# Kernel tuning notes

Hardware: AMD Instinct MI355X
Metric: run time of the kernel (lower is better)

The kernel has to match this reference:

```python
import jax, jax.numpy as jnp
import numpy as np

N, C, H, W = 512, 2048, 16, 8
NUM_CLASSES = 751
ALPHA = 1.2      # margin
LAMB = 0.5       # self.l
SIGMA = 0.8      # osm_sigma
BN_EPS = 1e-5


def setup_inputs() -> dict:
    key = jax.random.key(0)
    k1, k2, k3 = jax.random.split(key, 3)
    features = jax.random.normal(k1, (N, C, H, W), dtype=jnp.float32)
    targets = jax.random.randint(k2, (N,), 0, NUM_CLASSES)
    gamma = jnp.ones((C,), dtype=jnp.float32)  # BN weight, init 1 (weights_init_kaiming)
    # kaiming_uniform_(a=sqrt(5)) on [NUM_CLASSES, C]: bound = 1/sqrt(C)
    bound = 1.0 / np.sqrt(C)
    weight = jax.random.uniform(k3, (NUM_CLASSES, C), jnp.float32, -bound, bound)
    return {"features": features, "targets": targets, "gamma": gamma, "weight": weight}


def _l2norm(x, axis=-1):
    return x / jnp.maximum(jnp.linalg.norm(x, axis=axis, keepdims=True), 1e-12)


def reference(features, targets, gamma, weight):
    n = features.shape[0]
    # AdaptiveAvgPool2d(1) + Flatten
    global_feat = jnp.mean(features, axis=(2, 3))  # [n, C]
    # NoBiasBatchNorm1d (training mode: batch stats, biased var, no bias)
    mu = jnp.mean(global_feat, axis=0)
    var = jnp.var(global_feat, axis=0)
    bn_feat = (global_feat - mu) / jnp.sqrt(var + BN_EPS) * gamma
    bn_feat = _l2norm(bn_feat, axis=1)  # F.normalize

    # pairwise euclidean distance
    sq = jnp.sum(bn_feat * bn_feat, axis=1)                       # [n]
    dist2 = sq[:, None] + sq[None, :] - 2.0 * (bn_feat @ bn_feat.T)
    dist = jnp.sqrt(jnp.clip(dist2, 1e-12, None))                 # [n, n]

    S_pos = jnp.exp(-(dist * dist) / (SIGMA * SIGMA))
    S_neg = jnp.clip(ALPHA - dist, 1e-12, None)
    p_mask = targets[:, None] == targets[None, :]                 # [n, n] bool
    S = jnp.where(p_mask, S_pos, S_neg)

    # per-sample attention: exp(logits)[i, t_i] / sum_j exp(logits)[i, j] == softmax
    logits = bn_feat @ _l2norm(weight, axis=1).T                  # [n, num_classes]
    probs = jax.nn.softmax(logits, axis=1)
    atten = probs[jnp.arange(n), targets]                         # [n]
    A = jnp.minimum(atten[None, :], atten[:, None])               # [n, n]

    Wmat = S * A
    off_diag = 1.0 - jnp.eye(n, dtype=Wmat.dtype)
    W_P = Wmat * p_mask.astype(Wmat.dtype) * off_diag
    W_N = Wmat * (~p_mask).astype(Wmat.dtype) * off_diag

    L_P = 0.5 * jnp.sum(W_P * dist * dist) / jnp.sum(W_P)
    L_N = 0.5 * jnp.sum(W_N * S_neg * S_neg) / jnp.sum(W_N)
    L = (1.0 - LAMB) * L_P + LAMB * L_N
    return (L, global_feat)
```

## Files before the change

### kernel.cpp

```cpp
#include <hip/hip_runtime.h>
#include <hip/hip_bf16.h>
#include <math.h>

#define N_S   512
#define C_S   2048
#define HW_S  128
#define NCLS  751
#define NCLSP 768
#define ALPHA 1.2f
#define LAMB  0.5f
#define SIGMA 0.8f
#define BN_EPS 1e-5f

typedef __attribute__((ext_vector_type(8))) short short8;
typedef __attribute__((ext_vector_type(4))) float f32x4;

__device__ __forceinline__ unsigned short f2bf(float x) {
    __hip_bfloat16 h = __float2bfloat16(x);
    return *reinterpret_cast<unsigned short*>(&h);
}

__global__ __launch_bounds__(256) void pool_kernel(const float* __restrict__ feat,
                                                   float* __restrict__ out_gf,
                                                   float* __restrict__ accum) {
    if (blockIdx.x == 0 && threadIdx.x < 8) accum[threadIdx.x] = 0.0f;
    int pair = blockIdx.x * 16 + (threadIdx.x >> 4);
    int sub  = threadIdx.x & 15;
    const float4* p = reinterpret_cast<const float4*>(feat + (size_t)pair * HW_S);
    float4 v0 = p[sub];
    float4 v1 = p[sub + 16];
    float s = (v0.x + v0.y + v0.z + v0.w) + (v1.x + v1.y + v1.z + v1.w);
    #pragma unroll
    for (int off = 8; off > 0; off >>= 1) s += __shfl_down(s, off, 16);
    if (sub == 0) out_gf[pair] = s * (1.0f / HW_S);
}

__global__ __launch_bounds__(256) void meanvar_kernel(const float* __restrict__ gf,
                                                      const float* __restrict__ gamma,
                                                      float* __restrict__ mu_out,
                                                      float* __restrict__ scale_out) {
    int tc = threadIdx.x & 31;
    int tr = threadIdx.x >> 5;
    int c  = blockIdx.x * 32 + tc;
    const float* col = gf + c;
    float sum = 0.f, sumsq = 0.f;
    #pragma unroll 4
    for (int n = tr * 64; n < tr * 64 + 64; ++n) {
        float x = col[(size_t)n * C_S];
        sum += x; sumsq += x * x;
    }
    __shared__ float s1[8][32], s2[8][32];
    s1[tr][tc] = sum; s2[tr][tc] = sumsq;
    __syncthreads();
    if (threadIdx.x < 32) {
        int cc = blockIdx.x * 32 + threadIdx.x;
        float a = 0.f, b = 0.f;
        #pragma unroll
        for (int r = 0; r < 8; ++r) { a += s1[r][threadIdx.x]; b += s2[r][threadIdx.x]; }
        float mu  = a * (1.0f / N_S);
        float var = b * (1.0f / N_S) - mu * mu;
        mu_out[cc]    = mu;
        scale_out[cc] = gamma[cc] / sqrtf(var + BN_EPS);
    }
}

__global__ __launch_bounds__(256) void bnnorm_kernel(const float* __restrict__ gf,
                                                     const float* __restrict__ mu,
                                                     const float* __restrict__ scale,
                                                     unsigned short* __restrict__ bnnh,
                                                     float* __restrict__ sq) {
    int n = blockIdx.x, t = threadIdx.x;
    const float* row = gf + (size_t)n * C_S;
    float v[8];
    float ss = 0.f;
    #pragma unroll
    for (int k = 0; k < 8; ++k) {
        int c = t + k * 256;
        float x = (row[c] - mu[c]) * scale[c];
        v[k] = x; ss += x * x;
    }
    __shared__ float red[4];
    __shared__ float sinv;
    #pragma unroll
    for (int off = 32; off > 0; off >>= 1) ss += __shfl_down(ss, off, 64);
    if ((t & 63) == 0) red[t >> 6] = ss;
    __syncthreads();
    if (t == 0) {
        float tot = red[0] + red[1] + red[2] + red[3];
        float inv = 1.0f / fmaxf(sqrtf(tot), 1e-12f);
        sinv  = inv;
        sq[n] = tot * inv * inv;
    }
    __syncthreads();
    float inv = sinv;
    unsigned short* orow = bnnh + (size_t)n * C_S;
    #pragma unroll
    for (int k = 0; k < 8; ++k) orow[t + k * 256] = f2bf(v[k] * inv);
}

__global__ __launch_bounds__(256) void wnorm_kernel(const float* __restrict__ w,
                                                    unsigned short* __restrict__ wnh) {
    int kcls = blockIdx.x, t = threadIdx.x;
    unsigned short* orow = wnh + (size_t)kcls * C_S;
    if (kcls >= NCLS) {
        #pragma unroll
        for (int k = 0; k < 8; ++k) orow[t + k * 256] = 0;
        return;
    }
    const float* row = w + (size_t)kcls * C_S;
    float v[8];
    float ss = 0.f;
    #pragma unroll
    for (int k = 0; k < 8; ++k) {
        float x = row[t + k * 256];
        v[k] = x; ss += x * x;
    }
    __shared__ float red[4];
    __shared__ float sinv;
    #pragma unroll
    for (int off = 32; off > 0; off >>= 1) ss += __shfl_down(ss, off, 64);
    if ((t & 63) == 0) red[t >> 6] = ss;
    __syncthreads();
    if (t == 0) sinv = 1.0f / fmaxf(sqrtf(red[0] + red[1] + red[2] + red[3]), 1e-12f);
    __syncthreads();
    float inv = sinv;
    #pragma unroll
    for (int k = 0; k < 8; ++k) orow[t + k * 256] = f2bf(v[k] * inv);
}

__global__ __launch_bounds__(64) void mfma_gemm_nt(const unsigned short* __restrict__ Ah,
                                                   const unsigned short* __restrict__ Bh,
                                                   float* __restrict__ Cm,
                                                   int K, int ldc) {
    int lane = threadIdx.x & 63;
    int m0 = blockIdx.x * 16;
    int n0 = blockIdx.y * 64;
    int mrow = m0 + (lane & 15);
    int kq   = (lane >> 4) * 8;
    f32x4 acc0 = {0.f,0.f,0.f,0.f}, acc1 = {0.f,0.f,0.f,0.f};
    f32x4 acc2 = {0.f,0.f,0.f,0.f}, acc3 = {0.f,0.f,0.f,0.f};
    const unsigned short* arow = Ah + (size_t)mrow * K + kq;
    const unsigned short* brow = Bh + (size_t)(n0 + (lane & 15)) * K + kq;
    #pragma unroll 2
    for (int k = 0; k < K; k += 32) {
        short8 a  = *reinterpret_cast<const short8*>(arow + k);
        short8 b0 = *reinterpret_cast<const short8*>(brow + k);
        short8 b1 = *reinterpret_cast<const short8*>(brow + 16 * K + k);
        short8 b2 = *reinterpret_cast<const short8*>(brow + 32 * K + k);
        short8 b3 = *reinterpret_cast<const short8*>(brow + 48 * K + k);
        acc0 = __builtin_amdgcn_mfma_f32_16x16x32_bf16(a, b0, acc0, 0, 0, 0);
        acc1 = __builtin_amdgcn_mfma_f32_16x16x32_bf16(a, b1, acc1, 0, 0, 0);
        acc2 = __builtin_amdgcn_mfma_f32_16x16x32_bf16(a, b2, acc2, 0, 0, 0);
        acc3 = __builtin_amdgcn_mfma_f32_16x16x32_bf16(a, b3, acc3, 0, 0, 0);
    }
    int ccol  = lane & 15;
    int crow0 = m0 + (lane >> 4) * 4;
    #pragma unroll
    for (int r = 0; r < 4; ++r) {
        float* orow = Cm + (size_t)(crow0 + r) * ldc + n0 + ccol;
        orow[0]  = acc0[r];
        orow[16] = acc1[r];
        orow[32] = acc2[r];
        orow[48] = acc3[r];
    }
}

__global__ __launch_bounds__(256) void softmax_atten_kernel(const float* __restrict__ logits,
                                                            const int* __restrict__ targets,
                                                            float* __restrict__ atten) {
    int n = blockIdx.x, t = threadIdx.x;
    const float* row = logits + (size_t)n * NCLSP;
    __shared__ float red[4];
    __shared__ float srmax, srsum;
    float m = -1e30f;
    for (int k = t; k < NCLS; k += 256) m = fmaxf(m, row[k]);
    #pragma unroll
    for (int off = 32; off > 0; off >>= 1) m = fmaxf(m, __shfl_down(m, off, 64));
    if ((t & 63) == 0) red[t >> 6] = m;
    __syncthreads();
    if (t == 0) srmax = fmaxf(fmaxf(red[0], red[1]), fmaxf(red[2], red[3]));
    __syncthreads();
    float rm = srmax;
    float s = 0.f;
    for (int k = t; k < NCLS; k += 256) s += expf(row[k] - rm);
    #pragma unroll
    for (int off = 32; off > 0; off >>= 1) s += __shfl_down(s, off, 64);
    if ((t & 63) == 0) red[t >> 6] = s;
    __syncthreads();
    if (t == 0) {
        srsum = red[0] + red[1] + red[2] + red[3];
        atten[n] = expf(row[targets[n]] - rm) / srsum;
    }
}

__global__ __launch_bounds__(256) void pair_reduce_kernel(const float* __restrict__ G,
                                                          const float* __restrict__ sq,
                                                          const float* __restrict__ atten,
                                                          const int* __restrict__ targets,
                                                          float* __restrict__ accum,
                                                          float* __restrict__ out) {
    float numP = 0.f, denP = 0.f, numN = 0.f, denN = 0.f;
    const float inv_sig2 = 1.0f / (SIGMA * SIGMA);
    for (int p = blockIdx.x * 256 + threadIdx.x; p < N_S * N_S; p += 256 * 256) {
        int i = p >> 9, j = p & (N_S - 1);
        if (i == j) continue;
        float d2   = fmaxf(sq[i] + sq[j] - 2.0f * G[p], 1e-12f);
        float dist = sqrtf(d2);
        float sneg = fmaxf(ALPHA - dist, 1e-12f);
        float Aij  = fminf(atten[i], atten[j]);
        if (targets[i] == targets[j]) {
            float Wm = expf(-d2 * inv_sig2) * Aij;
            numP += Wm * d2; denP += Wm;
        } else {
            float Wm = sneg * Aij;
            numN += Wm * sneg * sneg; denN += Wm;
        }
    }
    #pragma unroll
    for (int off = 32; off > 0; off >>= 1) {
        numP += __shfl_down(numP, off, 64);
        denP += __shfl_down(denP, off, 64);
        numN += __shfl_down(numN, off, 64);
        denN += __shfl_down(denN, off, 64);
    }
    __shared__ float red[4][4];
    int t = threadIdx.x;
    if ((t & 63) == 0) {
        int w = t >> 6;
        red[w][0] = numP; red[w][1] = denP; red[w][2] = numN; red[w][3] = denN;
    }
    __syncthreads();
    if (t < 4) {
        float s = red[0][t] + red[1][t] + red[2][t] + red[3][t];
        atomicAdd(&accum[t], s);
    }
    __syncthreads();
    if (t == 0) {
        __threadfence();
        unsigned prev = atomicAdd(reinterpret_cast<unsigned*>(accum + 4), 1u);
        if (prev == gridDim.x - 1) {
            float a0 = atomicAdd(&accum[0], 0.0f);
            float a1 = atomicAdd(&accum[1], 0.0f);
            float a2 = atomicAdd(&accum[2], 0.0f);
            float a3 = atomicAdd(&accum[3], 0.0f);
            float L_P = 0.5f * a0 / a1;
            float L_N = 0.5f * a2 / a3;
            out[0] = (1.0f - LAMB) * L_P + LAMB * L_N;
        }
    }
}

extern "C" void kernel_launch(void* const* d_in, const int* in_sizes, int n_in,
                              void* d_out, int out_size, void* d_ws, size_t ws_size,
                              hipStream_t stream) {
    const float* features = (const float*)d_in[0];
    const int*   targets  = (const int*)d_in[1];
    const float* gamma    = (const float*)d_in[2];
    const float* weight   = (const float*)d_in[3];
    float* out = (float*)d_out;
    float* gf  = out + 1;

    float* ws     = (float*)d_ws;
    float* mu     = ws;
    float* scale  = mu + 2048;
    float* sq     = scale + 2048;
    float* atten  = sq + 512;
    float* accum  = atten + 512;
    float* logits = accum + 8;
    float* G      = logits + 393216;
    unsigned short* bnnh = (unsigned short*)(G + 262144);
    unsigned short* wnh  = bnnh + 1048576;

    hipLaunchKernelGGL(pool_kernel, dim3((N_S * C_S) / 16), dim3(256), 0, stream,
                       features, gf, accum);
    hipLaunchKernelGGL(meanvar_kernel, dim3(C_S / 32), dim3(256), 0, stream,
                       gf, gamma, mu, scale);
    hipLaunchKernelGGL(bnnorm_kernel, dim3(N_S), dim3(256), 0, stream,
                       gf, mu, scale, bnnh, sq);
    hipLaunchKernelGGL(wnorm_kernel, dim3(NCLSP), dim3(256), 0, stream, weight, wnh);
    hipLaunchKernelGGL(mfma_gemm_nt, dim3(N_S / 16, NCLSP / 64), dim3(64), 0, stream,
                       bnnh, wnh, logits, C_S, NCLSP);
    hipLaunchKernelGGL(softmax_atten_kernel, dim3(N_S), dim3(256), 0, stream,
                       logits, targets, atten);
    hipLaunchKernelGGL(mfma_gemm_nt, dim3(N_S / 16, N_S / 64), dim3(64), 0, stream,
                       bnnh, bnnh, G, C_S, N_S);
    hipLaunchKernelGGL(pair_reduce_kernel, dim3(256), dim3(256), 0, stream,
                       G, sq, atten, targets, accum, out);
}
```

Before: 746.9 us.

## Fuse post-pool stages into one persistent kernel with grid barriers

Replaces six separate kernel launches (mean/var, BN normalize, weight normalize, two GEMMs, softmax, pair reduce) with a single persistent kernel of 512 blocks that uses atomic-counter grid barriers between phases. Both GEMMs now run concurrently in one phase, and the pair reduction uses twice as many blocks. The aim is to remove launch overhead and inter-kernel gaps. The cost is spin-wait barriers, which rely on all 512 blocks being co-resident and can deadlock otherwise. Phases with fewer tasks than blocks also leave hardware idle.

```diff
diff --git a/kernel.cpp b/kernel.cpp
--- a/kernel.cpp
+++ b/kernel.cpp
@@ -11,6 +11,7 @@
 #define LAMB  0.5f
 #define SIGMA 0.8f
 #define BN_EPS 1e-5f
+#define NBLK  512
 
 typedef __attribute__((ext_vector_type(8))) short short8;
 typedef __attribute__((ext_vector_type(4))) float f32x4;
@@ -22,8 +23,8 @@
 
 __global__ __launch_bounds__(256) void pool_kernel(const float* __restrict__ feat,
                                                    float* __restrict__ out_gf,
-                                                   float* __restrict__ accum) {
-    if (blockIdx.x == 0 && threadIdx.x < 8) accum[threadIdx.x] = 0.0f;
+                                                   float* __restrict__ ctrl) {
+    if (blockIdx.x == 0 && threadIdx.x < 16) ctrl[threadIdx.x] = 0.0f;
     int pair = blockIdx.x * 16 + (threadIdx.x >> 4);
     int sub  = threadIdx.x & 15;
     const float4* p = reinterpret_cast<const float4*>(feat + (size_t)pair * HW_S);
@@ -35,217 +36,231 @@
     if (sub == 0) out_gf[pair] = s * (1.0f / HW_S);
 }
 
-__global__ __launch_bounds__(256) void meanvar_kernel(const float* __restrict__ gf,
-                                                      const float* __restrict__ gamma,
-                                                      float* __restrict__ mu_out,
-                                                      float* __restrict__ scale_out) {
-    int tc = threadIdx.x & 31;
-    int tr = threadIdx.x >> 5;
-    int c  = blockIdx.x * 32 + tc;
-    const float* col = gf + c;
-    float sum = 0.f, sumsq = 0.f;
-    #pragma unroll 4
-    for (int n = tr * 64; n < tr * 64 + 64; ++n) {
-        float x = col[(size_t)n * C_S];
-        sum += x; sumsq += x * x;
-    }
-    __shared__ float s1[8][32], s2[8][32];
-    s1[tr][tc] = sum; s2[tr][tc] = sumsq;
+__device__ __forceinline__ void grid_bar(unsigned* __restrict__ bars, int idx) {
     __syncthreads();
-    if (threadIdx.x < 32) {
-        int cc = blockIdx.x * 32 + threadIdx.x;
-        float a = 0.f, b = 0.f;
+    if (threadIdx.x == 0) {
+        __threadfence();
+        atomicAdd(&bars[idx], 1u);
+        while (atomicAdd(&bars[idx], 0u) < NBLK) __builtin_amdgcn_s_sleep(1);
+        __threadfence();
+    }
+    __syncthreads();
+}
+
+__global__ __launch_bounds__(256, 2) void fused_kernel(
+        const float* __restrict__ gf, const float* __restrict__ gamma,
+        const float* __restrict__ weight, const int* __restrict__ targets,
+        float* __restrict__ mu, float* __restrict__ scale,
+        float* __restrict__ sq, float* __restrict__ atten,
+        float* __restrict__ logits, float* __restrict__ G,
+        unsigned short* __restrict__ bnnh, unsigned short* __restrict__ wnh,
+        float* __restrict__ ctrl, float* __restrict__ out) {
+    const int t = threadIdx.x;
+    const int b = blockIdx.x;
+    unsigned* bars = reinterpret_cast<unsigned*>(ctrl + 8);
+
+    __shared__ float red1[8][32];
+    __shared__ float red2[8][32];
+    __shared__ float sred[4];
+    __shared__ float sbc[2];
+
+    if (b < 64) {
+        int tc = t & 31, tr = t >> 5;
+        int c = b * 32 + tc;
+        const float* col = gf + c;
+        float sum = 0.f, sumsq = 0.f;
+        #pragma unroll 4
+        for (int n = tr * 64; n < tr * 64 + 64; ++n) {
+            float x = col[(size_t)n * C_S];
+            sum += x; sumsq += x * x;
+        }
+        red1[tr][tc] = sum; red2[tr][tc] = sumsq;
+        __syncthreads();
+        if (t < 32) {
+            float a = 0.f, bb = 0.f;
+            #pragma unroll
+            for (int r = 0; r < 8; ++r) { a += red1[r][t]; bb += red2[r][t]; }
+            int cc = b * 32 + t;
+            float m   = a * (1.0f / N_S);
+            float var = bb * (1.0f / N_S) - m * m;
+            mu[cc]    = m;
+            scale[cc] = gamma[cc] / sqrtf(var + BN_EPS);
+        }
+    }
+    grid_bar(bars, 0);
+
+    for (int task = b; task < N_S + NCLSP; task += NBLK) {
+        __syncthreads();
+        if (task < N_S) {
+            int n = task;
+            const float* row = gf + (size_t)n * C_S;
+            float v[8]; float ss = 0.f;
+            #pragma unroll
+            for (int k = 0; k < 8; ++k) {
+                int c = t + k * 256;
+                float x = (row[c] - mu[c]) * scale[c];
+                v[k] = x; ss += x * x;
+            }
+            #pragma unroll
+            for (int off = 32; off > 0; off >>= 1) ss += __shfl_down(ss, off, 64);
+            if ((t & 63) == 0) sred[t >> 6] = ss;
+            __syncthreads();
+            if (t == 0) {
+                float tot = sred[0] + sred[1] + sred[2] + sred[3];
+                float inv = 1.0f / fmaxf(sqrtf(tot), 1e-12f);
+                sbc[0] = inv;
+                sq[n]  = tot * inv * inv;
+            }
+            __syncthreads();
+            float inv = sbc[0];
+            unsigned short* orow = bnnh + (size_t)n * C_S;
+            #pragma unroll
+            for (int k = 0; k < 8; ++k) orow[t + k * 256] = f2bf(v[k] * inv);
+        } else {
+            int r = task - N_S;
+            unsigned short* orow = wnh + (size_t)r * C_S;
+            if (r >= NCLS) {
+                #pragma unroll
+                for (int k = 0; k < 8; ++k) orow[t + k * 256] = 0;
+            } else {
+                const float* row = weight + (size_t)r * C_S;
+                float v[8]; float ss = 0.f;
+                #pragma unroll
+                for (int k = 0; k < 8; ++k) {
+                    float x = row[t + k * 256];
+                    v[k] = x; ss += x * x;
+                }
+                #pragma unroll
+                for (int off = 32; off > 0; off >>= 1) ss += __shfl_down(ss, off, 64);
+                if ((t & 63) == 0) sred[t >> 6] = ss;
+                __syncthreads();
+                if (t == 0) sbc[0] = 1.0f / fmaxf(sqrtf(sred[0]+sred[1]+sred[2]+sred[3]), 1e-12f);
+                __syncthreads();
+                float inv = sbc[0];
+                #pragma unroll
+                for (int k = 0; k < 8; ++k) orow[t + k * 256] = f2bf(v[k] * inv);
+            }
+        }
+    }
+    grid_bar(bars, 1);
+
+    {
+        int wave = t >> 6, lane = t & 63;
+        int gid = b * 4 + wave;
+        if (gid < 640) {
+            const unsigned short* Ah = bnnh;
+            const unsigned short* Bh; float* Cm; int m0, n0, ldc;
+            if (gid < 384) {
+                Bh = wnh;  Cm = logits; m0 = (gid & 31) * 16; n0 = (gid >> 5) * 64; ldc = NCLSP;
+            } else {
+                int g2 = gid - 384;
+                Bh = bnnh; Cm = G;      m0 = (g2 & 31) * 16;  n0 = (g2 >> 5) * 64;  ldc = N_S;
+            }
+            int mrow = m0 + (lane & 15);
+            int kq   = (lane >> 4) * 8;
+            f32x4 acc0 = {0,0,0,0}, acc1 = {0,0,0,0}, acc2 = {0,0,0,0}, acc3 = {0,0,0,0};
+            const unsigned short* arow = Ah + (size_t)mrow * C_S + kq;
+            const unsigned short* brow = Bh + (size_t)(n0 + (lane & 15)) * C_S + kq;
+            #pragma unroll 2
+            for (int k = 0; k < C_S; k += 32) {
+                short8 a  = *reinterpret_cast<const short8*>(arow + k);
+                short8 b0 = *reinterpret_cast<const short8*>(brow + k);
+                short8 b1 = *reinterpret_cast<const short8*>(brow + 16 * C_S + k);
+                short8 b2 = *reinterpret_cast<const short8*>(brow + 32 * C_S + k);
+                short8 b3 = *reinterpret_cast<const short8*>(brow + 48 * C_S + k);
+                acc0 = __builtin_amdgcn_mfma_f32_16x16x32_bf16(a, b0, acc0, 0, 0, 0);
+                acc1 = __builtin_amdgcn_mfma_f32_16x16x32_bf16(a, b1, acc1, 0, 0, 0);
+                acc2 = __builtin_amdgcn_mfma_f32_16x16x32_bf16(a, b2, acc2, 0, 0, 0);
+                acc3 = __builtin_amdgcn_mfma_f32_16x16x32_bf16(a, b3, acc3, 0, 0, 0);
+            }
+            int ccol  = lane & 15;
+            int crow0 = m0 + (lane >> 4) * 4;
+            #pragma unroll
+            for (int r = 0; r < 4; ++r) {
+                float* orow = Cm + (size_t)(crow0 + r) * ldc + n0 + ccol;
+                orow[0]  = acc0[r];
+                orow[16] = acc1[r];
+                orow[32] = acc2[r];
+                orow[48] = acc3[r];
+            }
+        }
+    }
+    grid_bar(bars, 2);
+
+    {
+        int n = b;
+        const float* row = logits + (size_t)n * NCLSP;
+        float m = -1e30f;
+        for (int k = t; k < NCLS; k += 256) m = fmaxf(m, row[k]);
         #pragma unroll
-        for (int r = 0; r < 8; ++r) { a += s1[r][threadIdx.x]; b += s2[r][threadIdx.x]; }
-        float mu  = a * (1.0f / N_S);
-        float var = b * (1.0f / N_S) - mu * mu;
-        mu_out[cc]    = mu;
-        scale_out[cc] = gamma[cc] / sqrtf(var + BN_EPS);
-    }
-}
-
-__global__ __launch_bounds__(256) void bnnorm_kernel(const float* __restrict__ gf,
-                                                     const float* __restrict__ mu,
-                                                     const float* __restrict__ scale,
-                                                     unsigned short* __restrict__ bnnh,
-                                                     float* __restrict__ sq) {
-    int n = blockIdx.x, t = threadIdx.x;
-    const float* row = gf + (size_t)n * C_S;
-    float v[8];
-    float ss = 0.f;
-    #pragma unroll
-    for (int k = 0; k < 8; ++k) {
-        int c = t + k * 256;
-        float x = (row[c] - mu[c]) * scale[c];
-        v[k] = x; ss += x * x;
-    }
-    __shared__ float red[4];
-    __shared__ float sinv;
-    #pragma unroll
-    for (int off = 32; off > 0; off >>= 1) ss += __shfl_down(ss, off, 64);
-    if ((t & 63) == 0) red[t >> 6] = ss;
-    __syncthreads();
-    if (t == 0) {
-        float tot = red[0] + red[1] + red[2] + red[3];
-        float inv = 1.0f / fmaxf(sqrtf(tot), 1e-12f);
-        sinv  = inv;
-        sq[n] = tot * inv * inv;
-    }
-    __syncthreads();
-    float inv = sinv;
-    unsigned short* orow = bnnh + (size_t)n * C_S;
-    #pragma unroll
-    for (int k = 0; k < 8; ++k) orow[t + k * 256] = f2bf(v[k] * inv);
-}
-
-__global__ __launch_bounds__(256) void wnorm_kernel(const float* __restrict__ w,
-                                                    unsigned short* __restrict__ wnh) {
-    int kcls = blockIdx.x, t = threadIdx.x;
-    unsigned short* orow = wnh + (size_t)kcls * C_S;
-    if (kcls >= NCLS) {
+        for (int off = 32; off > 0; off >>= 1) m = fmaxf(m, __shfl_down(m, off, 64));
+        if ((t & 63) == 0) sred[t >> 6] = m;
+        __syncthreads();
+        if (t == 0) sbc[0] = fmaxf(fmaxf(sred[0], sred[1]), fmaxf(sred[2], sred[3]));
+        __syncthreads();
+        float rm = sbc[0];
+        float s = 0.f;
+        for (int k = t; k < NCLS; k += 256) s += expf(row[k] - rm);
         #pragma unroll
-        for (int k = 0; k < 8; ++k) orow[t + k * 256] = 0;
-        return;
-    }
-    const float* row = w + (size_t)kcls * C_S;
-    float v[8];
-    float ss = 0.f;
-    #pragma unroll
-    for (int k = 0; k < 8; ++k) {
-        float x = row[t + k * 256];
-        v[k] = x; ss += x * x;
-    }
-    __shared__ float red[4];
-    __shared__ float sinv;
-    #pragma unroll
-    for (int off = 32; off > 0; off >>= 1) ss += __shfl_down(ss, off, 64);
-    if ((t & 63) == 0) red[t >> 6] = ss;
-    __syncthreads();
-    if (t == 0) sinv = 1.0f / fmaxf(sqrtf(red[0] + red[1] + red[2] + red[3]), 1e-12f);
-    __syncthreads();
-    float inv = sinv;
-    #pragma unroll
-    for (int k = 0; k < 8; ++k) orow[t + k * 256] = f2bf(v[k] * inv);
-}
-
-__global__ __launch_bounds__(64) void mfma_gemm_nt(const unsigned short* __restrict__ Ah,
-                                                   const unsigned short* __restrict__ Bh,
-                                                   float* __restrict__ Cm,
-                                                   int K, int ldc) {
-    int lane = threadIdx.x & 63;
-    int m0 = blockIdx.x * 16;
-    int n0 = blockIdx.y * 64;
-    int mrow = m0 + (lane & 15);
-    int kq   = (lane >> 4) * 8;
-    f32x4 acc0 = {0.f,0.f,0.f,0.f}, acc1 = {0.f,0.f,0.f,0.f};
-    f32x4 acc2 = {0.f,0.f,0.f,0.f}, acc3 = {0.f,0.f,0.f,0.f};
-    const unsigned short* arow = Ah + (size_t)mrow * K + kq;
-    const unsigned short* brow = Bh + (size_t)(n0 + (lane & 15)) * K + kq;
-    #pragma unroll 2
-    for (int k = 0; k < K; k += 32) {
-        short8 a  = *reinterpret_cast<const short8*>(arow + k);
-        short8 b0 = *reinterpret_cast<const short8*>(brow + k);
-        short8 b1 = *reinterpret_cast<const short8*>(brow + 16 * K + k);
-        short8 b2 = *reinterpret_cast<const short8*>(brow + 32 * K + k);
-        short8 b3 = *reinterpret_cast<const short8*>(brow + 48 * K + k);
-        acc0 = __builtin_amdgcn_mfma_f32_16x16x32_bf16(a, b0, acc0, 0, 0, 0);
-        acc1 = __builtin_amdgcn_mfma_f32_16x16x32_bf16(a, b1, acc1, 0, 0, 0);
-        acc2 = __builtin_amdgcn_mfma_f32_16x16x32_bf16(a, b2, acc2, 0, 0, 0);
-        acc3 = __builtin_amdgcn_mfma_f32_16x16x32_bf16(a, b3, acc3, 0, 0, 0);
-    }
-    int ccol  = lane & 15;
-    int crow0 = m0 + (lane >> 4) * 4;
-    #pragma unroll
-    for (int r = 0; r < 4; ++r) {
-        float* orow = Cm + (size_t)(crow0 + r) * ldc + n0 + ccol;
-        orow[0]  = acc0[r];
-        orow[16] = acc1[r];
-        orow[32] = acc2[r];
-        orow[48] = acc3[r];
-    }
-}
-
-__global__ __launch_bounds__(256) void softmax_atten_kernel(const float* __restrict__ logits,
-                                                            const int* __restrict__ targets,
-                                                            float* __restrict__ atten) {
-    int n = blockIdx.x, t = threadIdx.x;
-    const float* row = logits + (size_t)n * NCLSP;
-    __shared__ float red[4];
-    __shared__ float srmax, srsum;
-    float m = -1e30f;
-    for (int k = t; k < NCLS; k += 256) m = fmaxf(m, row[k]);
-    #pragma unroll
-    for (int off = 32; off > 0; off >>= 1) m = fmaxf(m, __shfl_down(m, off, 64));
-    if ((t & 63) == 0) red[t >> 6] = m;
-    __syncthreads();
-    if (t == 0) srmax = fmaxf(fmaxf(red[0], red[1]), fmaxf(red[2], red[3]));
-    __syncthreads();
-    float rm = srmax;
-    float s = 0.f;
-    for (int k = t; k < NCLS; k += 256) s += expf(row[k] - rm);
-    #pragma unroll
-    for (int off = 32; off > 0; off >>= 1) s += __shfl_down(s, off, 64);
-    if ((t & 63) == 0) red[t >> 6] = s;
-    __syncthreads();
-    if (t == 0) {
-        srsum = red[0] + red[1] + red[2] + red[3];
-        atten[n] = expf(row[targets[n]] - rm) / srsum;
-    }
-}
-
-__global__ __launch_bounds__(256) void pair_reduce_kernel(const float* __restrict__ G,
-                                                          const float* __restrict__ sq,
-                                                          const float* __restrict__ atten,
-                                                          const int* __restrict__ targets,
-                                                          float* __restrict__ accum,
-                                                          float* __restrict__ out) {
-    float numP = 0.f, denP = 0.f, numN = 0.f, denN = 0.f;
-    const float inv_sig2 = 1.0f / (SIGMA * SIGMA);
-    for (int p = blockIdx.x * 256 + threadIdx.x; p < N_S * N_S; p += 256 * 256) {
-        int i = p >> 9, j = p & (N_S - 1);
-        if (i == j) continue;
-        float d2   = fmaxf(sq[i] + sq[j] - 2.0f * G[p], 1e-12f);
-        float dist = sqrtf(d2);
-        float sneg = fmaxf(ALPHA - dist, 1e-12f);
-        float Aij  = fminf(atten[i], atten[j]);
-        if (targets[i] == targets[j]) {
-            float Wm = expf(-d2 * inv_sig2) * Aij;
-            numP += Wm * d2; denP += Wm;
-        } else {
-            float Wm = sneg * Aij;
-            numN += Wm * sneg * sneg; denN += Wm;
-        }
-    }
-    #pragma unroll
-    for (int off = 32; off > 0; off >>= 1) {
-        numP += __shfl_down(numP, off, 64);
-        denP += __shfl_down(denP, off, 64);
-        numN += __shfl_down(numN, off, 64);
-        denN += __shfl_down(denN, off, 64);
-    }
-    __shared__ float red[4][4];
-    int t = threadIdx.x;
-    if ((t & 63) == 0) {
-        int w = t >> 6;
-        red[w][0] = numP; red[w][1] = denP; red[w][2] = numN; red[w][3] = denN;
-    }
-    __syncthreads();
-    if (t < 4) {
-        float s = red[0][t] + red[1][t] + red[2][t] + red[3][t];
-        atomicAdd(&accum[t], s);
-    }
-    __syncthreads();
-    if (t == 0) {
-        __threadfence();
-        unsigned prev = atomicAdd(reinterpret_cast<unsigned*>(accum + 4), 1u);
-        if (prev == gridDim.x - 1) {
-            float a0 = atomicAdd(&accum[0], 0.0f);
-            float a1 = atomicAdd(&accum[1], 0.0f);
-            float a2 = atomicAdd(&accum[2], 0.0f);
-            float a3 = atomicAdd(&accum[3], 0.0f);
-            float L_P = 0.5f * a0 / a1;
-            float L_N = 0.5f * a2 / a3;
-            out[0] = (1.0f - LAMB) * L_P + LAMB * L_N;
+        for (int off = 32; off > 0; off >>= 1) s += __shfl_down(s, off, 64);
+        if ((t & 63) == 0) sred[t >> 6] = s;
+        __syncthreads();
+        if (t == 0) {
+            float ssum = sred[0] + sred[1] + sred[2] + sred[3];
+            atten[n] = expf(row[targets[n]] - rm) / ssum;
+        }
+    }
+    grid_bar(bars, 3);
+
+    {
+        float numP = 0.f, denP = 0.f, numN = 0.f, denN = 0.f;
+        const float inv_sig2 = 1.0f / (SIGMA * SIGMA);
+        for (int p = b * 256 + t; p < N_S * N_S; p += NBLK * 256) {
+            int i = p >> 9, j = p & (N_S - 1);
+            if (i == j) continue;
+            float d2   = fmaxf(sq[i] + sq[j] - 2.0f * G[p], 1e-12f);
+            float dist = sqrtf(d2);
+            float sneg = fmaxf(ALPHA - dist, 1e-12f);
+            float Aij  = fminf(atten[i], atten[j]);
+            if (targets[i] == targets[j]) {
+                float Wm = expf(-d2 * inv_sig2) * Aij;
+                numP += Wm * d2; denP += Wm;
+            } else {
+                float Wm = sneg * Aij;
+                numN += Wm * sneg * sneg; denN += Wm;
+            }
+        }
+        #pragma unroll
+        for (int off = 32; off > 0; off >>= 1) {
+            numP += __shfl_down(numP, off, 64);
+            denP += __shfl_down(denP, off, 64);
+            numN += __shfl_down(numN, off, 64);
+            denN += __shfl_down(denN, off, 64);
+        }
+        __syncthreads();
+        if ((t & 63) == 0) {
+            int w = t >> 6;
+            red1[0][w*4+0] = numP; red1[0][w*4+1] = denP;
+            red1[0][w*4+2] = numN; red1[0][w*4+3] = denN;
+        }
+        __syncthreads();
+        if (t < 4) {
+            float s = red1[0][t] + red1[0][4+t] + red1[0][8+t] + red1[0][12+t];
+            atomicAdd(&ctrl[t], s);
+        }
+        __syncthreads();
+        if (t == 0) {
+            __threadfence();
+            unsigned prev = atomicAdd(reinterpret_cast<unsigned*>(ctrl + 4), 1u);
+            if (prev == NBLK - 1) {
+                float a0 = atomicAdd(&ctrl[0], 0.0f);
+                float a1 = atomicAdd(&ctrl[1], 0.0f);
+                float a2 = atomicAdd(&ctrl[2], 0.0f);
+                float a3 = atomicAdd(&ctrl[3], 0.0f);
+                float L_P = 0.5f * a0 / a1;
+                float L_N = 0.5f * a2 / a3;
+                out[0] = (1.0f - LAMB) * L_P + LAMB * L_N;
+            }
         }
     }
 }
@@ -265,25 +280,15 @@
     float* scale  = mu + 2048;
     float* sq     = scale + 2048;
     float* atten  = sq + 512;
-    float* accum  = atten + 512;
-    float* logits = accum + 8;
+    float* ctrl   = atten + 512;
+    float* logits = ctrl + 16;
     float* G      = logits + 393216;
     unsigned short* bnnh = (unsigned short*)(G + 262144);
     unsigned short* wnh  = bnnh + 1048576;
 
     hipLaunchKernelGGL(pool_kernel, dim3((N_S * C_S) / 16), dim3(256), 0, stream,
-                       features, gf, accum);
-    hipLaunchKernelGGL(meanvar_kernel, dim3(C_S / 32), dim3(256), 0, stream,
-                       gf, gamma, mu, scale);
-    hipLaunchKernelGGL(bnnorm_kernel, dim3(N_S), dim3(256), 0, stream,
-                       gf, mu, scale, bnnh, sq);
-    hipLaunchKernelGGL(wnorm_kernel, dim3(NCLSP), dim3(256), 0, stream, weight, wnh);
-    hipLaunchKernelGGL(mfma_gemm_nt, dim3(N_S / 16, NCLSP / 64), dim3(64), 0, stream,
-                       bnnh, wnh, logits, C_S, NCLSP);
-    hipLaunchKernelGGL(softmax_atten_kernel, dim3(N_S), dim3(256), 0, stream,
-                       logits, targets, atten);
-    hipLaunchKernelGGL(mfma_gemm_nt, dim3(N_S / 16, N_S / 64), dim3(64), 0, stream,
-                       bnnh, bnnh, G, C_S, N_S);
-    hipLaunchKernelGGL(pair_reduce_kernel, dim3(256), dim3(256), 0, stream,
-                       G, sq, atten, targets, accum, out);
-}
+                       features, gf, ctrl);
+    hipLaunchKernelGGL(fused_kernel, dim3(NBLK), dim3(256), 0, stream,
+                       gf, gamma, weight, targets, mu, scale, sq, atten,
+                       logits, G, bnnh, wnh, ctrl, out);
+}
```

Result: slower. 903.7 us (+21.0%).

## Split-K both GEMMs in one launch, merge norm kernels, widen pool per-thread work

Applied to the files above, without the earlier changes.

The two bf16 MFMA GEMMs (logits and the Gram matrix) are merged into one 640-block launch with four waves per block. Each GEMM is split along K into four segments that write separate partial outputs. Softmax and the pair reduction then sum the four partials on read. The BN-normalise and weight-normalise kernels become a single launch, and the pooling kernel gives each thread twice as much data with a shorter shuffle reduction. The aim is more parallelism in the small GEMMs and fewer launches, at the cost of extra partial-output traffic and a larger workspace.

```diff
diff --git a/kernel.cpp b/kernel.cpp
--- a/kernel.cpp
+++ b/kernel.cpp
@@ -11,6 +11,8 @@
 #define LAMB  0.5f
 #define SIGMA 0.8f
 #define BN_EPS 1e-5f
+#define KSPLIT 4
+#define KSEG  (C_S / KSPLIT)
 
 typedef __attribute__((ext_vector_type(8))) short short8;
 typedef __attribute__((ext_vector_type(4))) float f32x4;
@@ -22,16 +24,19 @@
 
 __global__ __launch_bounds__(256) void pool_kernel(const float* __restrict__ feat,
                                                    float* __restrict__ out_gf,
-                                                   float* __restrict__ accum) {
-    if (blockIdx.x == 0 && threadIdx.x < 8) accum[threadIdx.x] = 0.0f;
-    int pair = blockIdx.x * 16 + (threadIdx.x >> 4);
-    int sub  = threadIdx.x & 15;
+                                                   float* __restrict__ ctrl) {
+    if (blockIdx.x == 0 && threadIdx.x < 8) ctrl[threadIdx.x] = 0.0f;
+    int pair = blockIdx.x * 32 + (threadIdx.x >> 3);
+    int sub  = threadIdx.x & 7;
     const float4* p = reinterpret_cast<const float4*>(feat + (size_t)pair * HW_S);
     float4 v0 = p[sub];
-    float4 v1 = p[sub + 16];
-    float s = (v0.x + v0.y + v0.z + v0.w) + (v1.x + v1.y + v1.z + v1.w);
-    #pragma unroll
-    for (int off = 8; off > 0; off >>= 1) s += __shfl_down(s, off, 16);
+    float4 v1 = p[sub + 8];
+    float4 v2 = p[sub + 16];
+    float4 v3 = p[sub + 24];
+    float s = (v0.x + v0.y + v0.z + v0.w) + (v1.x + v1.y + v1.z + v1.w)
+            + (v2.x + v2.y + v2.z + v2.w) + (v3.x + v3.y + v3.z + v3.w);
+    #pragma unroll
+    for (int off = 4; off > 0; off >>= 1) s += __shfl_down(s, off, 8);
     if (sub == 0) out_gf[pair] = s * (1.0f / HW_S);
 }
 
@@ -64,90 +69,98 @@
     }
 }
 
-__global__ __launch_bounds__(256) void bnnorm_kernel(const float* __restrict__ gf,
-                                                     const float* __restrict__ mu,
-                                                     const float* __restrict__ scale,
-                                                     unsigned short* __restrict__ bnnh,
-                                                     float* __restrict__ sq) {
-    int n = blockIdx.x, t = threadIdx.x;
-    const float* row = gf + (size_t)n * C_S;
-    float v[8];
-    float ss = 0.f;
-    #pragma unroll
-    for (int k = 0; k < 8; ++k) {
-        int c = t + k * 256;
-        float x = (row[c] - mu[c]) * scale[c];
-        v[k] = x; ss += x * x;
-    }
+__global__ __launch_bounds__(256) void norm_kernel(const float* __restrict__ gf,
+                                                   const float* __restrict__ mu,
+                                                   const float* __restrict__ scale,
+                                                   const float* __restrict__ w,
+                                                   unsigned short* __restrict__ bnnh,
+                                                   unsigned short* __restrict__ wnh,
+                                                   float* __restrict__ sq) {
+    int b = blockIdx.x, t = threadIdx.x;
     __shared__ float red[4];
     __shared__ float sinv;
-    #pragma unroll
-    for (int off = 32; off > 0; off >>= 1) ss += __shfl_down(ss, off, 64);
-    if ((t & 63) == 0) red[t >> 6] = ss;
-    __syncthreads();
-    if (t == 0) {
-        float tot = red[0] + red[1] + red[2] + red[3];
-        float inv = 1.0f / fmaxf(sqrtf(tot), 1e-12f);
-        sinv  = inv;
-        sq[n] = tot * inv * inv;
-    }
-    __syncthreads();
-    float inv = sinv;
-    unsigned short* orow = bnnh + (size_t)n * C_S;
-    #pragma unroll
-    for (int k = 0; k < 8; ++k) orow[t + k * 256] = f2bf(v[k] * inv);
-}
-
-__global__ __launch_bounds__(256) void wnorm_kernel(const float* __restrict__ w,
-                                                    unsigned short* __restrict__ wnh) {
-    int kcls = blockIdx.x, t = threadIdx.x;
-    unsigned short* orow = wnh + (size_t)kcls * C_S;
-    if (kcls >= NCLS) {
-        #pragma unroll
-        for (int k = 0; k < 8; ++k) orow[t + k * 256] = 0;
-        return;
-    }
-    const float* row = w + (size_t)kcls * C_S;
-    float v[8];
-    float ss = 0.f;
-    #pragma unroll
-    for (int k = 0; k < 8; ++k) {
-        float x = row[t + k * 256];
-        v[k] = x; ss += x * x;
-    }
-    __shared__ float red[4];
-    __shared__ float sinv;
-    #pragma unroll
-    for (int off = 32; off > 0; off >>= 1) ss += __shfl_down(ss, off, 64);
-    if ((t & 63) == 0) red[t >> 6] = ss;
-    __syncthreads();
-    if (t == 0) sinv = 1.0f / fmaxf(sqrtf(red[0] + red[1] + red[2] + red[3]), 1e-12f);
-    __syncthreads();
-    float inv = sinv;
-    #pragma unroll
-    for (int k = 0; k < 8; ++k) orow[t + k * 256] = f2bf(v[k] * inv);
-}
-
-__global__ __launch_bounds__(64) void mfma_gemm_nt(const unsigned short* __restrict__ Ah,
-                                                   const unsigned short* __restrict__ Bh,
-                                                   float* __restrict__ Cm,
-                                                   int K, int ldc) {
-    int lane = threadIdx.x & 63;
-    int m0 = blockIdx.x * 16;
-    int n0 = blockIdx.y * 64;
+    if (b < N_S) {
+        int n = b;
+        const float* row = gf + (size_t)n * C_S;
+        float v[8]; float ss = 0.f;
+        #pragma unroll
+        for (int k = 0; k < 8; ++k) {
+            int c = t + k * 256;
+            float x = (row[c] - mu[c]) * scale[c];
+            v[k] = x; ss += x * x;
+        }
+        #pragma unroll
+        for (int off = 32; off > 0; off >>= 1) ss += __shfl_down(ss, off, 64);
+        if ((t & 63) == 0) red[t >> 6] = ss;
+        __syncthreads();
+        if (t == 0) {
+            float tot = red[0] + red[1] + red[2] + red[3];
+            float inv = 1.0f / fmaxf(sqrtf(tot), 1e-12f);
+            sinv = inv;
+            sq[n] = tot * inv * inv;
+        }
+        __syncthreads();
+        float inv = sinv;
+        unsigned short* orow = bnnh + (size_t)n * C_S;
+        #pragma unroll
+        for (int k = 0; k < 8; ++k) orow[t + k * 256] = f2bf(v[k] * inv);
+    } else {
+        int r = b - N_S;
+        unsigned short* orow = wnh + (size_t)r * C_S;
+        if (r >= NCLS) {
+            #pragma unroll
+            for (int k = 0; k < 8; ++k) orow[t + k * 256] = 0;
+            return;
+        }
+        const float* row = w + (size_t)r * C_S;
+        float v[8]; float ss = 0.f;
+        #pragma unroll
+        for (int k = 0; k < 8; ++k) {
+            float x = row[t + k * 256];
+            v[k] = x; ss += x * x;
+        }
+        #pragma unroll
+        for (int off = 32; off > 0; off >>= 1) ss += __shfl_down(ss, off, 64);
+        if ((t & 63) == 0) red[t >> 6] = ss;
+        __syncthreads();
+        if (t == 0) sinv = 1.0f / fmaxf(sqrtf(red[0]+red[1]+red[2]+red[3]), 1e-12f);
+        __syncthreads();
+        float inv = sinv;
+        #pragma unroll
+        for (int k = 0; k < 8; ++k) orow[t + k * 256] = f2bf(v[k] * inv);
+    }
+}
+
+__global__ __launch_bounds__(256) void gemm_kernel(const unsigned short* __restrict__ bnnh,
+                                                   const unsigned short* __restrict__ wnh,
+                                                   float* __restrict__ logits_p,
+                                                   float* __restrict__ G_p) {
+    int wave = threadIdx.x >> 6, lane = threadIdx.x & 63;
+    int gid = blockIdx.x * 4 + wave;
+    const unsigned short* Bh; float* Cm; int m0, n0, ldc, ks;
+    if (gid < 1536) {
+        int tile = gid >> 2; ks = gid & 3;
+        Bh = wnh; m0 = (tile & 31) * 16; n0 = (tile >> 5) * 64; ldc = NCLSP;
+        Cm = logits_p + (size_t)ks * (N_S * NCLSP);
+    } else {
+        int g2 = gid - 1536;
+        int tile = g2 >> 2; ks = g2 & 3;
+        Bh = bnnh; m0 = (tile & 31) * 16; n0 = (tile >> 5) * 64; ldc = N_S;
+        Cm = G_p + (size_t)ks * (N_S * N_S);
+    }
+    int kbase = ks * KSEG;
     int mrow = m0 + (lane & 15);
     int kq   = (lane >> 4) * 8;
-    f32x4 acc0 = {0.f,0.f,0.f,0.f}, acc1 = {0.f,0.f,0.f,0.f};
-    f32x4 acc2 = {0.f,0.f,0.f,0.f}, acc3 = {0.f,0.f,0.f,0.f};
-    const unsigned short* arow = Ah + (size_t)mrow * K + kq;
-    const unsigned short* brow = Bh + (size_t)(n0 + (lane & 15)) * K + kq;
+    f32x4 acc0 = {0,0,0,0}, acc1 = {0,0,0,0}, acc2 = {0,0,0,0}, acc3 = {0,0,0,0};
+    const unsigned short* arow = bnnh + (size_t)mrow * C_S + kbase + kq;
+    const unsigned short* brow = Bh + (size_t)(n0 + (lane & 15)) * C_S + kbase + kq;
     #pragma unroll 2
-    for (int k = 0; k < K; k += 32) {
+    for (int k = 0; k < KSEG; k += 32) {
         short8 a  = *reinterpret_cast<const short8*>(arow + k);
         short8 b0 = *reinterpret_cast<const short8*>(brow + k);
-        short8 b1 = *reinterpret_cast<const short8*>(brow + 16 * K + k);
-        short8 b2 = *reinterpret_cast<const short8*>(brow + 32 * K + k);
-        short8 b3 = *reinterpret_cast<const short8*>(brow + 48 * K + k);
+        short8 b1 = *reinterpret_cast<const short8*>(brow + 16 * C_S + k);
+        short8 b2 = *reinterpret_cast<const short8*>(brow + 32 * C_S + k);
+        short8 b3 = *reinterpret_cast<const short8*>(brow + 48 * C_S + k);
         acc0 = __builtin_amdgcn_mfma_f32_16x16x32_bf16(a, b0, acc0, 0, 0, 0);
         acc1 = __builtin_amdgcn_mfma_f32_16x16x32_bf16(a, b1, acc1, 0, 0, 0);
         acc2 = __builtin_amdgcn_mfma_f32_16x16x32_bf16(a, b2, acc2, 0, 0, 0);
@@ -165,15 +178,18 @@
     }
 }
 
-__global__ __launch_bounds__(256) void softmax_atten_kernel(const float* __restrict__ logits,
+__global__ __launch_bounds__(256) void softmax_atten_kernel(const float* __restrict__ logits_p,
                                                             const int* __restrict__ targets,
                                                             float* __restrict__ atten) {
     int n = blockIdx.x, t = threadIdx.x;
-    const float* row = logits + (size_t)n * NCLSP;
+    const float* r0 = logits_p + (size_t)n * NCLSP;
+    const float* r1 = r0 + (size_t)(N_S * NCLSP);
+    const float* r2 = r1 + (size_t)(N_S * NCLSP);
+    const float* r3 = r2 + (size_t)(N_S * NCLSP);
     __shared__ float red[4];
     __shared__ float srmax, srsum;
     float m = -1e30f;
-    for (int k = t; k < NCLS; k += 256) m = fmaxf(m, row[k]);
+    for (int k = t; k < NCLS; k += 256) m = fmaxf(m, r0[k] + r1[k] + r2[k] + r3[k]);
     #pragma unroll
     for (int off = 32; off > 0; off >>= 1) m = fmaxf(m, __shfl_down(m, off, 64));
     if ((t & 63) == 0) red[t >> 6] = m;
@@ -182,29 +198,35 @@
     __syncthreads();
     float rm = srmax;
     float s = 0.f;
-    for (int k = t; k < NCLS; k += 256) s += expf(row[k] - rm);
+    for (int k = t; k < NCLS; k += 256) s += expf(r0[k] + r1[k] + r2[k] + r3[k] - rm);
     #pragma unroll
     for (int off = 32; off > 0; off >>= 1) s += __shfl_down(s, off, 64);
     if ((t & 63) == 0) red[t >> 6] = s;
     __syncthreads();
     if (t == 0) {
         srsum = red[0] + red[1] + red[2] + red[3];
-        atten[n] = expf(row[targets[n]] - rm) / srsum;
-    }
-}
-
-__global__ __launch_bounds__(256) void pair_reduce_kernel(const float* __restrict__ G,
+        int tg = targets[n];
+        atten[n] = expf(r0[tg] + r1[tg] + r2[tg] + r3[tg] - rm) / srsum;
+    }
+}
+
+__global__ __launch_bounds__(256) void pair_reduce_kernel(const float* __restrict__ G_p,
                                                           const float* __restrict__ sq,
                                                           const float* __restrict__ atten,
                                                           const int* __restrict__ targets,
-                                                          float* __restrict__ accum,
+                                                          float* __restrict__ ctrl,
                                                           float* __restrict__ out) {
     float numP = 0.f, denP = 0.f, numN = 0.f, denN = 0.f;
     const float inv_sig2 = 1.0f / (SIGMA * SIGMA);
+    const float* G0 = G_p;
+    const float* G1 = G0 + N_S * N_S;
+    const float* G2 = G1 + N_S * N_S;
+    const float* G3 = G2 + N_S * N_S;
     for (int p = blockIdx.x * 256 + threadIdx.x; p < N_S * N_S; p += 256 * 256) {
         int i = p >> 9, j = p & (N_S - 1);
         if (i == j) continue;
-        float d2   = fmaxf(sq[i] + sq[j] - 2.0f * G[p], 1e-12f);
+        float g    = G0[p] + G1[p] + G2[p] + G3[p];
+        float d2   = fmaxf(sq[i] + sq[j] - 2.0f * g, 1e-12f);
         float dist = sqrtf(d2);
         float sneg = fmaxf(ALPHA - dist, 1e-12f);
         float Aij  = fminf(atten[i], atten[j]);
@@ -232,17 +254,17 @@
     __syncthreads();
     if (t < 4) {
         float s = red[0][t] + red[1][t] + red[2][t] + red[3][t];
-        atomicAdd(&accum[t], s);
+        atomicAdd(&ctrl[t], s);
     }
     __syncthreads();
     if (t == 0) {
         __threadfence();
-        unsigned prev = atomicAdd(reinterpret_cast<unsigned*>(accum + 4), 1u);
+        unsigned prev = atomicAdd(reinterpret_cast<unsigned*>(ctrl + 4), 1u);
         if (prev == gridDim.x - 1) {
-            float a0 = atomicAdd(&accum[0], 0.0f);
-            float a1 = atomicAdd(&accum[1], 0.0f);
-            float a2 = atomicAdd(&accum[2], 0.0f);
-            float a3 = atomicAdd(&accum[3], 0.0f);
+            float a0 = atomicAdd(&ctrl[0], 0.0f);
+            float a1 = atomicAdd(&ctrl[1], 0.0f);
+            float a2 = atomicAdd(&ctrl[2], 0.0f);
+            float a3 = atomicAdd(&ctrl[3], 0.0f);
             float L_P = 0.5f * a0 / a1;
             float L_N = 0.5f * a2 / a3;
             out[0] = (1.0f - LAMB) * L_P + LAMB * L_N;
@@ -260,30 +282,27 @@
     float* out = (float*)d_out;
     float* gf  = out + 1;
 
-    float* ws     = (float*)d_ws;
-    float* mu     = ws;
-    float* scale  = mu + 2048;
-    float* sq     = scale + 2048;
-    float* atten  = sq + 512;
-    float* accum  = atten + 512;
-    float* logits = accum + 8;
-    float* G      = logits + 393216;
-    unsigned short* bnnh = (unsigned short*)(G + 262144);
-    unsigned short* wnh  = bnnh + 1048576;
-
-    hipLaunchKernelGGL(pool_kernel, dim3((N_S * C_S) / 16), dim3(256), 0, stream,
-                       features, gf, accum);
+    float* ws       = (float*)d_ws;
+    float* mu       = ws;
+    float* scale    = mu + 2048;
+    float* sq       = scale + 2048;
+    float* atten    = sq + 512;
+    float* ctrl     = atten + 512;
+    float* logits_p = ctrl + 16;
+    float* G_p      = logits_p + 4 * (N_S * NCLSP);
+    unsigned short* bnnh = (unsigned short*)(G_p + 4 * (N_S * N_S));
+    unsigned short* wnh  = bnnh + (size_t)N_S * C_S;
+
+    hipLaunchKernelGGL(pool_kernel, dim3((N_S * C_S) / 32), dim3(256), 0, stream,
+                       features, gf, ctrl);
     hipLaunchKernelGGL(meanvar_kernel, dim3(C_S / 32), dim3(256), 0, stream,
                        gf, gamma, mu, scale);
-    hipLaunchKernelGGL(bnnorm_kernel, dim3(N_S), dim3(256), 0, stream,
-                       gf, mu, scale, bnnh, sq);
-    hipLaunchKernelGGL(wnorm_kernel, dim3(NCLSP), dim3(256), 0, stream, weight, wnh);
-    hipLaunchKernelGGL(mfma_gemm_nt, dim3(N_S / 16, NCLSP / 64), dim3(64), 0, stream,
-                       bnnh, wnh, logits, C_S, NCLSP);
+    hipLaunchKernelGGL(norm_kernel, dim3(N_S + NCLSP), dim3(256), 0, stream,
+                       gf, mu, scale, weight, bnnh, wnh, sq);
+    hipLaunchKernelGGL(gemm_kernel, dim3(640), dim3(256), 0, stream,
+                       bnnh, wnh, logits_p, G_p);
     hipLaunchKernelGGL(softmax_atten_kernel, dim3(N_S), dim3(256), 0, stream,
-                       logits, targets, atten);
-    hipLaunchKernelGGL(mfma_gemm_nt, dim3(N_S / 16, N_S / 64), dim3(64), 0, stream,
-                       bnnh, bnnh, G, C_S, N_S);
+                       logits_p, targets, atten);
     hipLaunchKernelGGL(pair_reduce_kernel, dim3(256), dim3(256), 0, stream,
-                       G, sq, atten, targets, accum, out);
-}
+                       G_p, sq, atten, targets, ctrl, out);
+}
```

Result: no change. 734.3 us (-1.7%).
